# Optimization experiments

Hardware: AMD Instinct MI355X
Metric: run time of the kernel (lower is better)

The kernel has to match this reference:

```python
import jax, jax.numpy as jnp
import numpy as np

B, S = 4, 1024
H = 32
NOPE, ROPE, VDIM = 128, 64, 128
Q_LORA, KV_LORA = 1536, 512
SCALE = 1.0 / np.sqrt(NOPE + ROPE)


def _make_rope(total, d, dtype=jnp.float32):
    # gen_rope: theta_j = 10000^{-2j/d}, idx = pos * theta, tiled x2 -> (T,1,d)
    theta = 1.0 / (10000.0 ** (jnp.arange(0, d, 2, dtype=dtype) / d))
    idx = jnp.arange(total, dtype=dtype)[:, None] * theta[None, :]  # (T, d/2)
    idx = jnp.tile(idx, (1, 2))[:, None, :]                          # (T, 1, d)
    return jnp.cos(idx), jnp.sin(idx)


def _apply_rope(x, cos, sin):
    # x: (T, heads, d); cos/sin: (T, 1, d). Matches torch apply_rope:
    # deinterleave even/odd then rotate-half.
    d = x.shape[-1]
    xp = jnp.concatenate([x[..., 0::2], x[..., 1::2]], axis=-1)
    rot = jnp.concatenate([-xp[..., d // 2:], xp[..., : d // 2]], axis=-1)
    return xp * cos + rot * sin


def setup_inputs() -> dict:
    key = jax.random.key(0)
    ks = jax.random.split(key, 5)
    Q = jax.random.normal(ks[0], (B, S, Q_LORA), dtype=jnp.float32)
    KV = jax.random.normal(ks[1], (B, S, KV_LORA), dtype=jnp.float32)
    PE = jax.random.normal(ks[2], (B, S, ROPE), dtype=jnp.float32)
    WUQ = jax.random.normal(ks[3], (H * (NOPE + ROPE), Q_LORA), dtype=jnp.float32) / np.sqrt(Q_LORA)
    WUKV = jax.random.normal(ks[4], (H * (NOPE + VDIM), KV_LORA), dtype=jnp.float32) / np.sqrt(KV_LORA)
    cos, sin = _make_rope(B * S, ROPE)
    return {"Q": Q, "KV": KV, "PE": PE, "WUQ": WUQ, "WUKV": WUKV, "cos": cos, "sin": sin}


def reference(Q, KV, PE, WUQ, WUKV, cos, sin):
    # Up-project Q latent -> per-head (nope + rope) dims
    q = jnp.einsum('bsl,el->bse', Q, WUQ).reshape(B, S, H, NOPE + ROPE)
    q_nope, q_pe = q[..., :NOPE], q[..., NOPE:]
    q_pe = _apply_rope(q_pe.reshape(B * S, H, ROPE), cos, sin).reshape(B, S, H, ROPE)
    # Shared (per-token) rotary key part
    k_pe = _apply_rope(PE.reshape(B * S, 1, ROPE), cos, sin).reshape(B, S, 1, ROPE)
    # Up-project KV latent -> per-head (k_nope + v)
    kvu = jnp.einsum('bsl,el->bse', KV, WUKV).reshape(B, S, H, NOPE + VDIM)
    k_nope, v = kvu[..., :NOPE], kvu[..., NOPE:]
    q_full = jnp.concatenate([q_nope, q_pe], axis=-1)                      # (B,S,H,192)
    k_full = jnp.concatenate([k_nope, jnp.broadcast_to(k_pe, (B, S, H, ROPE))], axis=-1)
    scores = jnp.einsum('bqhd,bkhd->bhqk', q_full, k_full) * SCALE        # (B,H,S,S)
    causal = jnp.tril(jnp.ones((S, S), dtype=bool))
    scores = jnp.where(causal, scores, jnp.finfo(scores.dtype).min)
    attn = jax.nn.softmax(scores, axis=-1)
    out = jnp.einsum('bhqk,bkhd->bqhd', attn, v)                          # (B,S,H,VDIM)
    return out
```

## Files before the change

kernel.cpp:

```cpp
#include <hip/hip_runtime.h>
#include <hip/hip_bf16.h>


typedef __attribute__((ext_vector_type(8))) short s8v;
typedef __attribute__((ext_vector_type(4))) short s4v;
typedef __attribute__((ext_vector_type(4))) float f4v;

#define B_ 4
#define S_ 1024
#define H_ 32
#define SCALE_ 0.07216878364870322992f

__device__ __forceinline__ short f2bf(float f) {
  unsigned u = __builtin_bit_cast(unsigned, f);
  unsigned r = (u + 0x7FFFu + ((u >> 16) & 1u)) >> 16;
  return (short)(unsigned short)r;
}

__device__ __forceinline__ void gll16(const void* g, void* l) {
  __builtin_amdgcn_global_load_lds((const __attribute__((address_space(1))) void*)g,
                                   (__attribute__((address_space(3))) void*)l, 16, 0, 0);
}

__global__ __launch_bounds__(256) void convert_f32_bf16(const float* __restrict__ src,
                                                        short* __restrict__ dst, int n4) {
  int i = blockIdx.x * 256 + threadIdx.x;
  if (i >= n4) return;
  float4 v = reinterpret_cast<const float4*>(src)[i];
  s4v o;
  o[0] = f2bf(v.x); o[1] = f2bf(v.y); o[2] = f2bf(v.z); o[3] = f2bf(v.w);
  reinterpret_cast<s4v*>(dst)[i] = o;
}

template<int K, int MODE>
__global__ __launch_bounds__(256, 2) void gemm2p_kernel(
    const short* __restrict__ A, const short* __restrict__ Bt,
    const float* __restrict__ cosb, const float* __restrict__ sinb,
    short* __restrict__ out0, short* __restrict__ out1, int cpx) {
  constexpr int NT = K / 64;
  __shared__ short sA[3][128 * 64];
  __shared__ short sB[2][128 * 64];
  const int id = blockIdx.x;
  const int swz = (id & 7) * cpx + (id >> 3);
  const int m0 = (swz & 31) * 128;
  const int n0 = (swz >> 5) * 128;
  const int tid = threadIdx.x;
  const int w = tid >> 6, l = tid & 63;
  const int l15 = l & 15, lg = l >> 4;
  const int wr = (w >> 1) * 64, wc = (w & 1) * 64;
  const int rs7 = l15 & 7;
  f4v acc[4][4] = {};
  const int srow = tid >> 3;
  const int swsl = (tid & 7) ^ (srow & 7);
  const char* gA = (const char*)A + ((size_t)(m0 + srow) * K + swsl * 8) * 2;
  const char* gB = (const char*)Bt + ((size_t)(n0 + srow) * K + swsl * 8) * 2;
  const int ldst = tid * 16;

  auto stgA = [&](int buf, int kt) {
#pragma unroll
    for (int r4 = 0; r4 < 4; ++r4)
      gll16(gA + (size_t)r4 * (32 * K * 2) + kt * 128, (char*)sA[buf] + r4 * 4096 + ldst);
  };
  auto stgB = [&](int buf, int kt) {
#pragma unroll
    for (int r4 = 0; r4 < 4; ++r4)
      gll16(gB + (size_t)r4 * (32 * K * 2) + kt * 128, (char*)sB[buf] + r4 * 4096 + ldst);
  };

  stgA(0, 0); stgB(0, 0);
  stgA(1, 1); stgB(1, 1);
  asm volatile("s_waitcnt vmcnt(8)" ::: "memory");
  __builtin_amdgcn_sched_barrier(0);
  __builtin_amdgcn_s_barrier();

  int a3 = 0;
  for (int v = 0; v < NT; ++v) {
    const char* bufA = (const char*)sA[a3];
    const char* bufB = (const char*)sB[v & 1];
    s8v bf[2][4];
#pragma unroll
    for (int kc = 0; kc < 2; ++kc)
#pragma unroll
      for (int n = 0; n < 4; ++n)
        bf[kc][n] = *(const s8v*)(bufB + (wc + n * 16 + l15) * 128 + (((kc * 4 + lg) ^ rs7) << 4));
    asm volatile("s_waitcnt lgkmcnt(0)" ::: "memory");
    __builtin_amdgcn_sched_barrier(0);
    __builtin_amdgcn_s_barrier();
    const bool stg = (v + 2 < NT);
    if (stg) {
      int a2 = a3 + 2; if (a2 >= 3) a2 -= 3;
      stgA(a2, v + 2);
      stgB(v & 1, v + 2);
    }
    __builtin_amdgcn_s_setprio(1);
#pragma unroll
    for (int kc = 0; kc < 2; ++kc)
#pragma unroll
      for (int i = 0; i < 4; ++i) {
        s8v af = *(const s8v*)(bufA + (wr + i * 16 + l15) * 128 + (((kc * 4 + lg) ^ rs7) << 4));
#pragma unroll
        for (int n = 0; n < 4; ++n)
          acc[i][n] = __builtin_amdgcn_mfma_f32_16x16x32_bf16(af, bf[kc][n], acc[i][n], 0, 0, 0);
      }
    __builtin_amdgcn_s_setprio(0);
    if (stg) asm volatile("s_waitcnt vmcnt(8)" ::: "memory");
    else     asm volatile("s_waitcnt vmcnt(0)" ::: "memory");
    __builtin_amdgcn_sched_barrier(0);
    __builtin_amdgcn_s_barrier();
    a3 = (a3 == 2) ? 0 : a3 + 1;
  }

#pragma unroll
  for (int j = 0; j < 4; ++j) {
    const int colb = n0 + wc + j * 16;
    if (MODE == 0) {
      const int e0 = colb % 192;
      const int h = colb / 192;
      const int e = e0 + l15;
      const bool is_pe = (e0 >= 128);
#pragma unroll
      for (int i = 0; i < 4; ++i) {
#pragma unroll
        for (int r = 0; r < 4; ++r) {
          const int row = m0 + wr + i * 16 + lg * 4 + r;
          const int b = row >> 10, s = row & 1023;
          const size_t base = ((size_t)(b * H_ + h) * S_ + s) * 192;
          float val = acc[i][j][r] * SCALE_;
          if (!is_pe) {
            out0[base + e] = f2bf(val);
          } else {
            float other = __shfl_xor(val, 1, 64);
            int p = (e - 128) >> 1;
            float cv = cosb[(size_t)row * 64 + p];
            float sv = sinb[(size_t)row * 64 + p];
            float o = ((l & 1) == 0) ? (val * cv - other * sv) : (val * cv + other * sv);
            int ep = ((l & 1) == 0) ? (128 + p) : (160 + p);
            out0[base + ep] = f2bf(o);
          }
        }
      }
    } else {
      const int e0 = colb % 256;
      const int h = colb / 256;
      const int e = e0 + l15;
      const bool is_v = (e0 >= 128);
#pragma unroll
      for (int i = 0; i < 4; ++i) {
#pragma unroll
        for (int r = 0; r < 4; ++r) {
          const int row = m0 + wr + i * 16 + lg * 4 + r;
          const int b = row >> 10, s = row & 1023;
          float val = acc[i][j][r];
          if (!is_v) {
            out0[((size_t)(b * H_ + h) * S_ + s) * 192 + e] = f2bf(val);
          } else {
            out1[((size_t)(b * H_ + h) * 128 + (e - 128)) * S_ + s] = f2bf(val);
          }
        }
      }
    }
  }
}

__global__ __launch_bounds__(64) void kpe_kernel(const float* __restrict__ PE,
                                                 const float* __restrict__ cosb,
                                                 const float* __restrict__ sinb,
                                                 short* __restrict__ kfull) {
  const int pos = blockIdx.x;
  const int t = threadIdx.x;
  const int p = t & 31;
  float x0 = PE[(size_t)pos * 64 + 2 * p];
  float x1 = PE[(size_t)pos * 64 + 2 * p + 1];
  float cv = cosb[(size_t)pos * 64 + p];
  float sv = sinb[(size_t)pos * 64 + p];
  float o = (t < 32) ? (x0 * cv - x1 * sv) : (x1 * cv + x0 * sv);
  short ob = f2bf(o);
  const int b = pos >> 10, s = pos & 1023;
#pragma unroll
  for (int h = 0; h < H_; ++h)
    kfull[(((size_t)b * H_ + h) * S_ + s) * 192 + 128 + t] = ob;
}

__global__ __launch_bounds__(256, 2) void attn_kernel(
    const short* __restrict__ qfull, const short* __restrict__ kfull,
    const short* __restrict__ vt, float* __restrict__ out) {
  __shared__ short sK[2][64 * 192];
  const int bid = blockIdx.x;
  const int qb = 7 - (bid >> 7);
  const int bh = bid & 127;
  const int b = bh >> 5, h = bh & 31;
  const int tid = threadIdx.x;
  const int w = tid >> 6, l = tid & 63;
  const int l15 = l & 15, lg = l >> 4;
  const short* Qh = qfull + (size_t)bh * (S_ * 192);
  const char*  KhB = (const char*)(kfull + (size_t)bh * (S_ * 192));
  const short* Vh = vt + (size_t)bh * (128 * S_);
  const int qw = qb * 128 + w * 32;

  s8v qfr[2][6];
#pragma unroll
  for (int mq = 0; mq < 2; ++mq)
#pragma unroll
    for (int kc = 0; kc < 6; ++kc)
      qfr[mq][kc] = *reinterpret_cast<const s8v*>(
          &Qh[(size_t)(qw + mq * 16 + l15) * 192 + kc * 32 + lg * 8]);

  unsigned kOff[6];
#pragma unroll
  for (int c = 0; c < 6; ++c) {
    unsigned o = (unsigned)(w * 6 + c) * 1024u + (unsigned)l * 16u;
    unsigned row = o / 384u;
    unsigned cb = o - row * 384u;
    kOff[c] = row * 384u + (cb ^ ((row & 7u) << 4));
  }

#pragma unroll
  for (int c = 0; c < 6; ++c)
    gll16(KhB + kOff[c], (char*)(&sK[0][0]) + (w * 6 + c) * 1024);
  __syncthreads();

  f4v acc[8][2] = {};
  float mrun[2] = {-3.0e38f, -3.0e38f};
  float lsum[2] = {0.f, 0.f};
  const int nt = 2 * (qb + 1);
  int cur = 0;
  for (int t = 0; t < nt; ++t) {
    const int k0 = t * 64;
    if (t + 1 < nt) {
      const char* gb = KhB + (size_t)(t + 1) * (64 * 384);
      char* lb = (char*)(&sK[cur ^ 1][0]);
#pragma unroll
      for (int c = 0; c < 6; ++c)
        gll16(gb + kOff[c], lb + (w * 6 + c) * 1024);
    }
    if (k0 <= qw + 31) {
      const char* sKc = (const char*)(&sK[cur][0]);
      f4v s[4][2] = {};
#pragma unroll
      for (int T = 0; T < 4; ++T) {
        const int row = T * 16 + l15;
        const unsigned swz = (unsigned)((row & 7) << 4);
#pragma unroll
        for (int kc = 0; kc < 6; ++kc) {
          s8v kf = *reinterpret_cast<const s8v*>(
              sKc + row * 384 + (unsigned)((kc * 64 + lg * 16) ^ swz));
          s[T][0] = __builtin_amdgcn_mfma_f32_16x16x32_bf16(kf, qfr[0][kc], s[T][0], 0, 0, 0);
          s[T][1] = __builtin_amdgcn_mfma_f32_16x16x32_bf16(kf, qfr[1][kc], s[T][1], 0, 0, 0);
        }
      }
      const bool diag = (t >= 2 * qb);
      unsigned pk[4][2][2];
#pragma unroll
      for (int mq = 0; mq < 2; ++mq) {
        const int qlane = qw + mq * 16 + l15;
        if (diag) {
#pragma unroll
          for (int T = 0; T < 4; ++T)
#pragma unroll
            for (int r = 0; r < 4; ++r)
              if (k0 + T * 16 + lg * 4 + r > qlane) s[T][mq][r] = -1.0e30f;
        }
        float tmax = s[0][mq][0];
#pragma unroll
        for (int T = 0; T < 4; ++T)
#pragma unroll
          for (int r = 0; r < 4; ++r) tmax = fmaxf(tmax, s[T][mq][r]);
        tmax = fmaxf(tmax, __shfl_xor(tmax, 16, 64));
        tmax = fmaxf(tmax, __shfl_xor(tmax, 32, 64));
        const float mnew = fmaxf(mrun[mq], tmax);
        const float cf = __expf(mrun[mq] - mnew);
        mrun[mq] = mnew;
        float rs = 0.f;
#pragma unroll
        for (int T = 0; T < 4; ++T)
#pragma unroll
          for (int r = 0; r < 4; ++r) {
            float e = __expf(s[T][mq][r] - mnew);
            s[T][mq][r] = e;
            rs += e;
          }
        rs += __shfl_xor(rs, 16, 64);
        rs += __shfl_xor(rs, 32, 64);
        lsum[mq] = lsum[mq] * cf + rs;
#pragma unroll
        for (int dt = 0; dt < 8; ++dt)
#pragma unroll
          for (int r = 0; r < 4; ++r) acc[dt][mq][r] *= cf;
#pragma unroll
        for (int T = 0; T < 4; ++T) {
          pk[T][mq][0] = (unsigned)(unsigned short)f2bf(s[T][mq][0]) |
                         ((unsigned)(unsigned short)f2bf(s[T][mq][1]) << 16);
          pk[T][mq][1] = (unsigned)(unsigned short)f2bf(s[T][mq][2]) |
                         ((unsigned)(unsigned short)f2bf(s[T][mq][3]) << 16);
        }
      }
#pragma unroll
      for (int c2 = 0; c2 < 2; ++c2) {
        union { unsigned u[4]; s8v v; } bb[2];
#pragma unroll
        for (int mq = 0; mq < 2; ++mq)
#pragma unroll
          for (int j2 = 0; j2 < 4; ++j2) {
            int src = l15 + ((l & 16) << 1) + ((j2 & 2) << 3);
            unsigned va = (unsigned)__shfl((int)pk[2 * c2][mq][j2 & 1], src, 64);
            unsigned vb = (unsigned)__shfl((int)pk[2 * c2 + 1][mq][j2 & 1], src, 64);
            bb[mq].u[j2] = (l & 32) ? vb : va;
          }
#pragma unroll
        for (int dt = 0; dt < 8; ++dt) {
          s8v vf = *reinterpret_cast<const s8v*>(
              &Vh[(size_t)(dt * 16 + l15) * S_ + k0 + c2 * 32 + lg * 8]);
          acc[dt][0] = __builtin_amdgcn_mfma_f32_16x16x32_bf16(vf, bb[0].v, acc[dt][0], 0, 0, 0);
          acc[dt][1] = __builtin_amdgcn_mfma_f32_16x16x32_bf16(vf, bb[1].v, acc[dt][1], 0, 0, 0);
        }
      }
    }
    __syncthreads();
    cur ^= 1;
  }
#pragma unroll
  for (int mq = 0; mq < 2; ++mq) {
    const float inv = 1.0f / lsum[mq];
    const int q = qw + mq * 16 + l15;
    float* ob = out + (((size_t)b * S_ + q) * H_ + h) * 128 + lg * 4;
#pragma unroll
    for (int dt = 0; dt < 8; ++dt) {
      float4 o4 = { acc[dt][mq][0] * inv, acc[dt][mq][1] * inv,
                    acc[dt][mq][2] * inv, acc[dt][mq][3] * inv };
      *reinterpret_cast<float4*>(ob + dt * 16) = o4;
    }
  }
}

extern "C" void kernel_launch(void* const* d_in, const int* in_sizes, int n_in,
                              void* d_out, int out_size, void* d_ws, size_t ws_size,
                              hipStream_t stream) {
  const float* Q    = (const float*)d_in[0];
  const float* KV   = (const float*)d_in[1];
  const float* PE   = (const float*)d_in[2];
  const float* WUQ  = (const float*)d_in[3];
  const float* WUKV = (const float*)d_in[4];
  const float* cosb = (const float*)d_in[5];
  const float* sinb = (const float*)d_in[6];
  float* out = (float*)d_out;
  char* ws = (char*)d_ws;

  short* Qb    = (short*)(ws);
  short* Wq    = (short*)(ws + 12582912);
  short* KVb   = (short*)(ws + 31457280);
  short* Wkv   = (short*)(ws + 35651584);
  short* qfull = (short*)(ws + 44040192);
  short* kfull = (short*)(ws + 94371840);
  short* vtb   = (short*)(ws + 144703488);

  convert_f32_bf16<<<6144, 256, 0, stream>>>(Q, Qb, 1572864);
  convert_f32_bf16<<<9216, 256, 0, stream>>>(WUQ, Wq, 2359296);
  convert_f32_bf16<<<2048, 256, 0, stream>>>(KV, KVb, 524288);
  convert_f32_bf16<<<4096, 256, 0, stream>>>(WUKV, Wkv, 1048576);

  gemm2p_kernel<1536, 0><<<1536, 256, 0, stream>>>(Qb, Wq, cosb, sinb, qfull, nullptr, 192);
  gemm2p_kernel<512, 1><<<2048, 256, 0, stream>>>(KVb, Wkv, nullptr, nullptr, kfull, vtb, 256);
  kpe_kernel<<<4096, 64, 0, stream>>>(PE, cosb, sinb, kfull);

  attn_kernel<<<1024, 256, 0, stream>>>(qfull, kfull, vtb, out);
}
```

Measured before the change: 348.4 us.

## Fuse conversions, rope and both GEMMs into fewer launches; lazy softmax rescale

Result: faster. 314.3 us (-9.8%).

```diff
diff --git a/kernel.cpp b/kernel.cpp
--- a/kernel.cpp
+++ b/kernel.cpp
@@ -22,28 +22,49 @@
                                    (__attribute__((address_space(3))) void*)l, 16, 0, 0);
 }
 
-__global__ __launch_bounds__(256) void convert_f32_bf16(const float* __restrict__ src,
-                                                        short* __restrict__ dst, int n4) {
-  int i = blockIdx.x * 256 + threadIdx.x;
-  if (i >= n4) return;
-  float4 v = reinterpret_cast<const float4*>(src)[i];
-  s4v o;
-  o[0] = f2bf(v.x); o[1] = f2bf(v.y); o[2] = f2bf(v.z); o[3] = f2bf(v.w);
-  reinterpret_cast<s4v*>(dst)[i] = o;
+__global__ __launch_bounds__(256) void prep_kernel(
+    const float* __restrict__ Q, const float* __restrict__ WUQ,
+    const float* __restrict__ KV, const float* __restrict__ WUKV,
+    const float* __restrict__ PE, const float* __restrict__ cosb,
+    const float* __restrict__ sinb,
+    short* __restrict__ Qb, short* __restrict__ Wq,
+    short* __restrict__ KVb, short* __restrict__ Wkv,
+    short* __restrict__ kfull) {
+  const int b = blockIdx.x;
+  if (b < 21504) {
+    int i = b * 256 + threadIdx.x;
+    const float* src; short* dst;
+    if (i < 1572864)      { src = Q;    dst = Qb; }
+    else if (i < 3932160) { src = WUQ;  dst = Wq;  i -= 1572864; }
+    else if (i < 4456448) { src = KV;   dst = KVb; i -= 3932160; }
+    else                  { src = WUKV; dst = Wkv; i -= 4456448; }
+    float4 v = reinterpret_cast<const float4*>(src)[i];
+    s4v o;
+    o[0] = f2bf(v.x); o[1] = f2bf(v.y); o[2] = f2bf(v.z); o[3] = f2bf(v.w);
+    reinterpret_cast<s4v*>(dst)[i] = o;
+  } else {
+    const int pos = (b - 21504) * 4 + (threadIdx.x >> 6);
+    const int t = threadIdx.x & 63;
+    const int p = t & 31;
+    float x0 = PE[(size_t)pos * 64 + 2 * p];
+    float x1 = PE[(size_t)pos * 64 + 2 * p + 1];
+    float cv = cosb[(size_t)pos * 64 + p];
+    float sv = sinb[(size_t)pos * 64 + p];
+    float o = (t < 32) ? (x0 * cv - x1 * sv) : (x1 * cv + x0 * sv);
+    short ob = f2bf(o);
+    const int bb = pos >> 10, s = pos & 1023;
+#pragma unroll
+    for (int h = 0; h < H_; ++h)
+      kfull[(((size_t)bb * H_ + h) * S_ + s) * 192 + 128 + t] = ob;
+  }
 }
 
 template<int K, int MODE>
-__global__ __launch_bounds__(256, 2) void gemm2p_kernel(
-    const short* __restrict__ A, const short* __restrict__ Bt,
-    const float* __restrict__ cosb, const float* __restrict__ sinb,
-    short* __restrict__ out0, short* __restrict__ out1, int cpx) {
-  constexpr int NT = K / 64;
-  __shared__ short sA[3][128 * 64];
-  __shared__ short sB[2][128 * 64];
-  const int id = blockIdx.x;
-  const int swz = (id & 7) * cpx + (id >> 3);
-  const int m0 = (swz & 31) * 128;
-  const int n0 = (swz >> 5) * 128;
+__device__ __forceinline__ void gemm_body(
+    const int m0, const int n0, const short* __restrict__ A,
+    const short* __restrict__ Bt, const float* __restrict__ cosb,
+    const float* __restrict__ sinb, short* __restrict__ out0,
+    short* __restrict__ out1, char* sAb, char* sBb) {
   const int tid = threadIdx.x;
   const int w = tid >> 6, l = tid & 63;
   const int l15 = l & 15, lg = l >> 4;
@@ -56,58 +77,39 @@
   const char* gB = (const char*)Bt + ((size_t)(n0 + srow) * K + swsl * 8) * 2;
   const int ldst = tid * 16;
 
-  auto stgA = [&](int buf, int kt) {
-#pragma unroll
-    for (int r4 = 0; r4 < 4; ++r4)
-      gll16(gA + (size_t)r4 * (32 * K * 2) + kt * 128, (char*)sA[buf] + r4 * 4096 + ldst);
-  };
-  auto stgB = [&](int buf, int kt) {
-#pragma unroll
-    for (int r4 = 0; r4 < 4; ++r4)
-      gll16(gB + (size_t)r4 * (32 * K * 2) + kt * 128, (char*)sB[buf] + r4 * 4096 + ldst);
-  };
-
-  stgA(0, 0); stgB(0, 0);
-  stgA(1, 1); stgB(1, 1);
-  asm volatile("s_waitcnt vmcnt(8)" ::: "memory");
-  __builtin_amdgcn_sched_barrier(0);
-  __builtin_amdgcn_s_barrier();
-
-  int a3 = 0;
-  for (int v = 0; v < NT; ++v) {
-    const char* bufA = (const char*)sA[a3];
-    const char* bufB = (const char*)sB[v & 1];
-    s8v bf[2][4];
-#pragma unroll
-    for (int kc = 0; kc < 2; ++kc)
-#pragma unroll
-      for (int n = 0; n < 4; ++n)
-        bf[kc][n] = *(const s8v*)(bufB + (wc + n * 16 + l15) * 128 + (((kc * 4 + lg) ^ rs7) << 4));
-    asm volatile("s_waitcnt lgkmcnt(0)" ::: "memory");
-    __builtin_amdgcn_sched_barrier(0);
-    __builtin_amdgcn_s_barrier();
-    const bool stg = (v + 2 < NT);
-    if (stg) {
-      int a2 = a3 + 2; if (a2 >= 3) a2 -= 3;
-      stgA(a2, v + 2);
-      stgB(v & 1, v + 2);
-    }
-    __builtin_amdgcn_s_setprio(1);
-#pragma unroll
-    for (int kc = 0; kc < 2; ++kc)
-#pragma unroll
-      for (int i = 0; i < 4; ++i) {
-        s8v af = *(const s8v*)(bufA + (wr + i * 16 + l15) * 128 + (((kc * 4 + lg) ^ rs7) << 4));
-#pragma unroll
-        for (int n = 0; n < 4; ++n)
-          acc[i][n] = __builtin_amdgcn_mfma_f32_16x16x32_bf16(af, bf[kc][n], acc[i][n], 0, 0, 0);
-      }
-    __builtin_amdgcn_s_setprio(0);
-    if (stg) asm volatile("s_waitcnt vmcnt(8)" ::: "memory");
-    else     asm volatile("s_waitcnt vmcnt(0)" ::: "memory");
-    __builtin_amdgcn_sched_barrier(0);
-    __builtin_amdgcn_s_barrier();
-    a3 = (a3 == 2) ? 0 : a3 + 1;
+#pragma unroll
+  for (int r4 = 0; r4 < 4; ++r4) {
+    gll16(gA + (size_t)r4 * (32 * K * 2), sAb + r4 * 4096 + ldst);
+    gll16(gB + (size_t)r4 * (32 * K * 2), sBb + r4 * 4096 + ldst);
+  }
+
+  int cur = 0;
+  for (int kk = 0; kk < K; kk += 64) {
+    __syncthreads();
+    if (kk + 64 < K) {
+      const char* ga = gA + (size_t)(kk + 64) * 2;
+      const char* gb = gB + (size_t)(kk + 64) * 2;
+#pragma unroll
+      for (int r4 = 0; r4 < 4; ++r4) {
+        gll16(ga + (size_t)r4 * (32 * K * 2), sAb + (cur ^ 1) * 16384 + r4 * 4096 + ldst);
+        gll16(gb + (size_t)r4 * (32 * K * 2), sBb + (cur ^ 1) * 16384 + r4 * 4096 + ldst);
+      }
+    }
+#pragma unroll
+    for (int kc = 0; kc < 2; ++kc) {
+      s8v af[4], bfv[4];
+#pragma unroll
+      for (int x = 0; x < 4; ++x) {
+        af[x]  = *(const s8v*)(sAb + cur * 16384 + (wr + x * 16 + l15) * 128 + (((kc * 4 + lg) ^ rs7) << 4));
+        bfv[x] = *(const s8v*)(sBb + cur * 16384 + (wc + x * 16 + l15) * 128 + (((kc * 4 + lg) ^ rs7) << 4));
+      }
+#pragma unroll
+      for (int i = 0; i < 4; ++i)
+#pragma unroll
+        for (int j = 0; j < 4; ++j)
+          acc[i][j] = __builtin_amdgcn_mfma_f32_16x16x32_bf16(af[i], bfv[j], acc[i][j], 0, 0, 0);
+    }
+    cur ^= 1;
   }
 
 #pragma unroll
@@ -162,23 +164,27 @@
   }
 }
 
-__global__ __launch_bounds__(64) void kpe_kernel(const float* __restrict__ PE,
-                                                 const float* __restrict__ cosb,
-                                                 const float* __restrict__ sinb,
-                                                 short* __restrict__ kfull) {
-  const int pos = blockIdx.x;
-  const int t = threadIdx.x;
-  const int p = t & 31;
-  float x0 = PE[(size_t)pos * 64 + 2 * p];
-  float x1 = PE[(size_t)pos * 64 + 2 * p + 1];
-  float cv = cosb[(size_t)pos * 64 + p];
-  float sv = sinb[(size_t)pos * 64 + p];
-  float o = (t < 32) ? (x0 * cv - x1 * sv) : (x1 * cv + x0 * sv);
-  short ob = f2bf(o);
-  const int b = pos >> 10, s = pos & 1023;
-#pragma unroll
-  for (int h = 0; h < H_; ++h)
-    kfull[(((size_t)b * H_ + h) * S_ + s) * 192 + 128 + t] = ob;
+__global__ __launch_bounds__(256, 2) void gemm_fused(
+    const short* __restrict__ Qb, const short* __restrict__ Wq,
+    const short* __restrict__ KVb, const short* __restrict__ Wkv,
+    const float* __restrict__ cosb, const float* __restrict__ sinb,
+    short* __restrict__ qfull, short* __restrict__ kfull,
+    short* __restrict__ vtb) {
+  __shared__ char sAb[2 * 16384];
+  __shared__ char sBb[2 * 16384];
+  const int id = blockIdx.x;
+  if (id < 1536) {
+    const int xcd = id & 7, j = id >> 3;
+    const int m0 = (xcd * 4 + (j & 3)) * 128;
+    const int n0 = (j >> 2) * 128;
+    gemm_body<1536, 0>(m0, n0, Qb, Wq, cosb, sinb, qfull, nullptr, sAb, sBb);
+  } else {
+    const int idp = id - 1536;
+    const int xcd = idp & 7, j = idp >> 3;
+    const int m0 = (xcd * 4 + (j & 3)) * 128;
+    const int n0 = (j >> 2) * 128;
+    gemm_body<512, 1>(m0, n0, KVb, Wkv, nullptr, nullptr, kfull, vtb, sAb, sBb);
+  }
 }
 
 __global__ __launch_bounds__(256, 2) void attn_kernel(
@@ -226,6 +232,14 @@
   int cur = 0;
   for (int t = 0; t < nt; ++t) {
     const int k0 = t * 64;
+    const bool compute = (k0 <= qw + 31);
+    s8v vf0[8];
+    if (compute) {
+#pragma unroll
+      for (int dt = 0; dt < 8; ++dt)
+        vf0[dt] = *reinterpret_cast<const s8v*>(
+            &Vh[(size_t)(dt * 16 + l15) * S_ + k0 + lg * 8]);
+    }
     if (t + 1 < nt) {
       const char* gb = KhB + (size_t)(t + 1) * (64 * 384);
       char* lb = (char*)(&sK[cur ^ 1][0]);
@@ -233,7 +247,7 @@
       for (int c = 0; c < 6; ++c)
         gll16(gb + kOff[c], lb + (w * 6 + c) * 1024);
     }
-    if (k0 <= qw + 31) {
+    if (compute) {
       const char* sKc = (const char*)(&sK[cur][0]);
       f4v s[4][2] = {};
 #pragma unroll
@@ -267,25 +281,28 @@
           for (int r = 0; r < 4; ++r) tmax = fmaxf(tmax, s[T][mq][r]);
         tmax = fmaxf(tmax, __shfl_xor(tmax, 16, 64));
         tmax = fmaxf(tmax, __shfl_xor(tmax, 32, 64));
-        const float mnew = fmaxf(mrun[mq], tmax);
-        const float cf = __expf(mrun[mq] - mnew);
-        mrun[mq] = mnew;
+        if (!__all(tmax <= mrun[mq] + 8.0f)) {
+          const float mnew = fmaxf(mrun[mq], tmax);
+          const float cf = __expf(mrun[mq] - mnew);
+          mrun[mq] = mnew;
+          lsum[mq] *= cf;
+#pragma unroll
+          for (int dt = 0; dt < 8; ++dt)
+#pragma unroll
+            for (int r = 0; r < 4; ++r) acc[dt][mq][r] *= cf;
+        }
         float rs = 0.f;
 #pragma unroll
         for (int T = 0; T < 4; ++T)
 #pragma unroll
           for (int r = 0; r < 4; ++r) {
-            float e = __expf(s[T][mq][r] - mnew);
+            float e = __expf(s[T][mq][r] - mrun[mq]);
             s[T][mq][r] = e;
             rs += e;
           }
         rs += __shfl_xor(rs, 16, 64);
         rs += __shfl_xor(rs, 32, 64);
-        lsum[mq] = lsum[mq] * cf + rs;
-#pragma unroll
-        for (int dt = 0; dt < 8; ++dt)
-#pragma unroll
-          for (int r = 0; r < 4; ++r) acc[dt][mq][r] *= cf;
+        lsum[mq] += rs;
 #pragma unroll
         for (int T = 0; T < 4; ++T) {
           pk[T][mq][0] = (unsigned)(unsigned short)f2bf(s[T][mq][0]) |
@@ -308,10 +325,11 @@
           }
 #pragma unroll
         for (int dt = 0; dt < 8; ++dt) {
-          s8v vf = *reinterpret_cast<const s8v*>(
-              &Vh[(size_t)(dt * 16 + l15) * S_ + k0 + c2 * 32 + lg * 8]);
-          acc[dt][0] = __builtin_amdgcn_mfma_f32_16x16x32_bf16(vf, bb[0].v, acc[dt][0], 0, 0, 0);
-          acc[dt][1] = __builtin_amdgcn_mfma_f32_16x16x32_bf16(vf, bb[1].v, acc[dt][1], 0, 0, 0);
+          s8v vfx = (c2 == 0) ? vf0[dt]
+                              : *reinterpret_cast<const s8v*>(
+                                    &Vh[(size_t)(dt * 16 + l15) * S_ + k0 + 32 + lg * 8]);
+          acc[dt][0] = __builtin_amdgcn_mfma_f32_16x16x32_bf16(vfx, bb[0].v, acc[dt][0], 0, 0, 0);
+          acc[dt][1] = __builtin_amdgcn_mfma_f32_16x16x32_bf16(vfx, bb[1].v, acc[dt][1], 0, 0, 0);
         }
       }
     }
@@ -353,14 +371,9 @@
   short* kfull = (short*)(ws + 94371840);
   short* vtb   = (short*)(ws + 144703488);
 
-  convert_f32_bf16<<<6144, 256, 0, stream>>>(Q, Qb, 1572864);
-  convert_f32_bf16<<<9216, 256, 0, stream>>>(WUQ, Wq, 2359296);
-  convert_f32_bf16<<<2048, 256, 0, stream>>>(KV, KVb, 524288);
-  convert_f32_bf16<<<4096, 256, 0, stream>>>(WUKV, Wkv, 1048576);
-
-  gemm2p_kernel<1536, 0><<<1536, 256, 0, stream>>>(Qb, Wq, cosb, sinb, qfull, nullptr, 192);
-  gemm2p_kernel<512, 1><<<2048, 256, 0, stream>>>(KVb, Wkv, nullptr, nullptr, kfull, vtb, 256);
-  kpe_kernel<<<4096, 64, 0, stream>>>(PE, cosb, sinb, kfull);
-
+  prep_kernel<<<22528, 256, 0, stream>>>(Q, WUQ, KV, WUKV, PE, cosb, sinb,
+                                         Qb, Wq, KVb, Wkv, kfull);
+  gemm_fused<<<3584, 256, 0, stream>>>(Qb, Wq, KVb, Wkv, cosb, sinb,
+                                       qfull, kfull, vtb);
   attn_kernel<<<1024, 256, 0, stream>>>(qfull, kfull, vtb, out);
 }
```
